# Optimization experiments

Measured on AMD Instinct MI355X. Metric: run time of the kernel, lower is better.

Reference implementation:

```python
import math
import jax, jax.numpy as jnp
import numpy as np

B, H, S, D = 2, 16, 2048, 1024
DK = D // H  # 64


def setup_inputs() -> dict:
    key = jax.random.key(0)
    k1, k2, k3, k4, k5 = jax.random.split(key, 5)
    scale = np.float32(0.02)
    return {
        "x": jax.random.normal(k1, (B, H, S, D), dtype=jnp.float32),
        "wq": jax.random.normal(k2, (DK, D), dtype=jnp.float32) * scale,
        "wk": jax.random.normal(k3, (DK, D), dtype=jnp.float32) * scale,
        "wv": jax.random.normal(k4, (DK, D), dtype=jnp.float32) * scale,
        "wo": jax.random.normal(k5, (D, D), dtype=jnp.float32) * scale,
    }


def reference(x, wq, wk, wv, wo):
    # x: [B, H, S, D]; wq/wk/wv: [dk, D]; wo: [D, D]
    b, h, s, d = x.shape
    xq = jnp.einsum("bhsd,kd->bhsk", x, wq)  # [B,H,S,dk]
    xk = jnp.einsum("bhsd,kd->bhsk", x, wk)
    xv = jnp.einsum("bhsd,kd->bhsk", x, wv)
    # NOTE: original scales by sqrt(hidden_dim), not sqrt(dk)
    inv_scale = np.float32(1.0 / math.sqrt(d))
    score = jnp.einsum("bhsk,bhtk->bhst", xq, xk) * inv_scale  # [B,H,S,S]
    attn = jax.nn.softmax(score, axis=-1).astype(xq.dtype)
    out = jnp.einsum("bhst,bhtk->bhsk", attn, xv)  # [B,H,S,dk]
    out = out.transpose(0, 2, 1, 3).reshape(b, s, h * (wq.shape[0]))  # [B,S,H*dk]
    return out @ wo.T  # [B,S,D]
```

## Files before the change

### kernel.cpp

```cpp
#include <hip/hip_runtime.h>
#include <math.h>

#define BB 2
#define HH 16
#define SS 2048
#define DD 1024
#define DK 64
#define BHS (BB*HH*SS)
#define QSCALE 0.04508422f

typedef short  bf16x8  __attribute__((ext_vector_type(8)));
typedef float  floatx4 __attribute__((ext_vector_type(4)));
typedef unsigned short u16;

#define MFMA(a,b,c) __builtin_amdgcn_mfma_f32_16x16x32_bf16((a),(b),(c),0,0,0)

__device__ __forceinline__ unsigned cvt_pk_bf16(float lo, float hi) {
    unsigned r;
    asm("v_cvt_pk_bf16_f32 %0, %1, %2" : "=v"(r) : "v"(lo), "v"(hi));
    return r;
}
__device__ __forceinline__ bf16x8 ldfrag(const u16* p) {
    union { uint4 u; bf16x8 b; } c;
    c.u = *(const uint4*)p;
    return c.b;
}
__device__ __forceinline__ void stbf4(u16* p, float4 t) {
    union { unsigned u[2]; uint2 v; } c;
    c.u[0] = cvt_pk_bf16(t.x, t.y);
    c.u[1] = cvt_pk_bf16(t.z, t.w);
    *(uint2*)p = c.v;
}
__device__ __forceinline__ void st4s(u16* p, float a, float b, float c, float d) {
    unsigned x = cvt_pk_bf16(a, b), y = cvt_pk_bf16(c, d);
    p[0]  = (u16)x; p[16] = (u16)(x >> 16);
    p[32] = (u16)y; p[48] = (u16)(y >> 16);
}

#define WQKV_CHUNKS (192*1024/4)
#define WO_CHUNKS   (1024*1024/4)
__global__ __launch_bounds__(256) void convert_w(
    const float* __restrict__ wq, const float* __restrict__ wk,
    const float* __restrict__ wv, const float* __restrict__ wo,
    u16* __restrict__ wqkv, u16* __restrict__ wo_bf)
{
    int i = blockIdx.x * 256 + threadIdx.x;
    if (i < WQKV_CHUNKS) {
        int r = i >> 8;
        int c = i & 255;
        const float* src = (r < 64) ? wq : ((r < 128) ? wk : wv);
        float4 t = *(const float4*)(src + (size_t)(r & 63) * DD + c * 4);
        stbf4(wqkv + (size_t)r * DD + c * 4, t);
    } else if (i < WQKV_CHUNKS + WO_CHUNKS) {
        int j = i - WQKV_CHUNKS;
        float4 t = *(const float4*)(wo + (size_t)j * 4);
        stbf4(wo_bf + (size_t)j * 4, t);
    }
}

__global__ __launch_bounds__(256) void qkv_proj(
    const float* __restrict__ x, const u16* __restrict__ wqkv,
    u16* __restrict__ q, u16* __restrict__ k, u16* __restrict__ vT)
{
    __shared__ __align__(16) u16 Xs[64][72];
    __shared__ __align__(16) u16 Ws[192][72];
    const int tid  = threadIdx.x;
    const int w    = tid >> 6;
    const int lane = tid & 63;
    const int quad = lane >> 4;
    const int l16  = lane & 15;
    const int rowbase = blockIdx.x * 64;

    floatx4 acc[12];
#pragma unroll
    for (int n = 0; n < 12; ++n) acc[n] = (floatx4){0.f,0.f,0.f,0.f};

    for (int k0 = 0; k0 < DD; k0 += 64) {
#pragma unroll
        for (int it = 0; it < 4; ++it) {
            int li = tid + it * 256;
            int r  = li >> 4;
            int c4 = li & 15;
            float4 t = *(const float4*)(x + (size_t)(rowbase + r) * DD + k0 + c4 * 4);
            stbf4(&Xs[r][c4 * 4], t);
        }
#pragma unroll
        for (int it = 0; it < 6; ++it) {
            int li = tid + it * 256;
            int r  = li >> 3;
            int c8 = li & 7;
            *(uint4*)&Ws[r][c8 * 8] =
                *(const uint4*)(wqkv + (size_t)r * DD + k0 + c8 * 8);
        }
        __syncthreads();

        bf16x8 a0 = ldfrag(&Xs[w * 16 + l16][quad * 8]);
        bf16x8 a1 = ldfrag(&Xs[w * 16 + l16][32 + quad * 8]);
#pragma unroll
        for (int n = 0; n < 12; ++n) {
            bf16x8 b0 = ldfrag(&Ws[n * 16 + l16][quad * 8]);
            bf16x8 b1 = ldfrag(&Ws[n * 16 + l16][32 + quad * 8]);
            acc[n] = MFMA(a0, b0, acc[n]);
            acc[n] = MFMA(a1, b1, acc[n]);
        }
        __syncthreads();
    }

#pragma unroll
    for (int r = 0; r < 4; ++r) {
        int row = w * 16 + quad * 4 + r;
        size_t m = (size_t)(rowbase + row);
        st4s(&q[m * DK + l16], acc[0][r] * QSCALE, acc[1][r] * QSCALE,
                               acc[2][r] * QSCALE, acc[3][r] * QSCALE);
        st4s(&k[m * DK + l16], acc[4][r], acc[5][r], acc[6][r], acc[7][r]);
    }
    u16 (*Vbuf)[72] = Xs;
#pragma unroll
    for (int r = 0; r < 4; ++r) {
        int row = w * 16 + quad * 4 + r;
        st4s(&Vbuf[row][l16], acc[8][r], acc[9][r], acc[10][r], acc[11][r]);
    }
    __syncthreads();
    {
        const int dk = tid >> 2;
        const int sc = (tid & 3) * 16;
        const int bh = rowbase >> 11;
        const int s0 = rowbase & 2047;
        union { u16 s[16]; uint4 u[2]; } t;
#pragma unroll
        for (int u = 0; u < 16; ++u) t.s[u] = Vbuf[sc + u][dk];
        uint4* dst = (uint4*)(vT + ((size_t)(bh * DK + dk)) * SS + s0 + sc);
        dst[0] = t.u[0];
        dst[1] = t.u[1];
    }
}

__global__ __launch_bounds__(256) void flash_attn(
    const u16* __restrict__ q, const u16* __restrict__ k,
    const u16* __restrict__ vT, u16* __restrict__ ao)
{
    __shared__ __align__(16) u16 Qs[64][72];
    __shared__ __align__(16) u16 Ks[64][72];
    __shared__ __align__(16) u16 Vt[64][72];
    __shared__ __align__(16) u16 Ps[4][16][72];
    const int tid  = threadIdx.x;
    const int w    = tid >> 6;
    const int lane = tid & 63;
    const int quad = lane >> 4;
    const int l16  = lane & 15;
    const int qt   = blockIdx.x;
    const int bh   = blockIdx.y;
    const size_t kbase = (size_t)bh * SS * DK;
    const size_t vbase = (size_t)bh * DK * SS;

#pragma unroll
    for (int it = 0; it < 2; ++it) {
        int li = tid + it * 256;
        int r  = li >> 3;
        int c8 = li & 7;
        *(uint4*)&Qs[r][c8 * 8] =
            *(const uint4*)(q + kbase + (size_t)(qt * 64 + r) * DK + c8 * 8);
    }

    float m_i[4], l_i[4];
    floatx4 acc_o[4];
#pragma unroll
    for (int r = 0; r < 4; ++r) { m_i[r] = -INFINITY; l_i[r] = 0.f; }
#pragma unroll
    for (int n = 0; n < 4; ++n) acc_o[n] = (floatx4){0.f,0.f,0.f,0.f};
    __syncthreads();

    for (int kt = 0; kt < SS / 64; ++kt) {
#pragma unroll
        for (int it = 0; it < 2; ++it) {
            int li = tid + it * 256;
            int r  = li >> 3;
            int c8 = li & 7;
            *(uint4*)&Ks[r][c8 * 8] =
                *(const uint4*)(k + kbase + (size_t)(kt * 64 + r) * DK + c8 * 8);
            *(uint4*)&Vt[r][c8 * 8] =
                *(const uint4*)(vT + vbase + (size_t)r * SS + kt * 64 + c8 * 8);
        }
        __syncthreads();

        floatx4 sc[4];
        __builtin_amdgcn_s_setprio(1);
        {
            bf16x8 a0 = ldfrag(&Qs[w * 16 + l16][quad * 8]);
            bf16x8 a1 = ldfrag(&Qs[w * 16 + l16][32 + quad * 8]);
#pragma unroll
            for (int n = 0; n < 4; ++n) {
                sc[n] = (floatx4){0.f,0.f,0.f,0.f};
                bf16x8 b0 = ldfrag(&Ks[n * 16 + l16][quad * 8]);
                bf16x8 b1 = ldfrag(&Ks[n * 16 + l16][32 + quad * 8]);
                sc[n] = MFMA(a0, b0, sc[n]);
                sc[n] = MFMA(a1, b1, sc[n]);
            }
        }
        __builtin_amdgcn_s_setprio(0);

        float rmx[4];
#pragma unroll
        for (int r = 0; r < 4; ++r) {
            float rm = fmaxf(fmaxf(sc[0][r], sc[1][r]), fmaxf(sc[2][r], sc[3][r]));
#pragma unroll
            for (int off = 1; off < 16; off <<= 1)
                rm = fmaxf(rm, __shfl_xor(rm, off, 64));
            rmx[r] = rm;
        }
        int ok = (rmx[0] <= m_i[0] + 8.f) & (rmx[1] <= m_i[1] + 8.f) &
                 (rmx[2] <= m_i[2] + 8.f) & (rmx[3] <= m_i[3] + 8.f);
        if (!__all(ok)) {
#pragma unroll
            for (int r = 0; r < 4; ++r) {
                float mnew  = fmaxf(m_i[r], rmx[r]);
                float alpha = __builtin_amdgcn_exp2f(m_i[r] - mnew);
#pragma unroll
                for (int n = 0; n < 4; ++n) acc_o[n][r] *= alpha;
                l_i[r] *= alpha;
                m_i[r]  = mnew;
            }
        }
#pragma unroll
        for (int r = 0; r < 4; ++r) {
            float mi = m_i[r];
            float p0 = __builtin_amdgcn_exp2f(sc[0][r] - mi);
            float p1 = __builtin_amdgcn_exp2f(sc[1][r] - mi);
            float p2 = __builtin_amdgcn_exp2f(sc[2][r] - mi);
            float p3 = __builtin_amdgcn_exp2f(sc[3][r] - mi);
            float rs = (p0 + p1) + (p2 + p3);
#pragma unroll
            for (int off = 1; off < 16; off <<= 1)
                rs += __shfl_xor(rs, off, 64);
            l_i[r] += rs;
            st4s(&Ps[w][quad * 4 + r][l16], p0, p1, p2, p3);
        }

        __builtin_amdgcn_s_setprio(1);
#pragma unroll
        for (int kc = 0; kc < 2; ++kc) {
            bf16x8 a = ldfrag(&Ps[w][l16][kc * 32 + quad * 8]);
#pragma unroll
            for (int n = 0; n < 4; ++n) {
                bf16x8 b = ldfrag(&Vt[n * 16 + l16][kc * 32 + quad * 8]);
                acc_o[n] = MFMA(a, b, acc_o[n]);
            }
        }
        __builtin_amdgcn_s_setprio(0);
        __syncthreads();
    }

    const int b = bh >> 4, h = bh & 15;
#pragma unroll
    for (int r = 0; r < 4; ++r) {
        int srow = qt * 64 + w * 16 + quad * 4 + r;
        float rl = __builtin_amdgcn_rcpf(l_i[r]);
        size_t base = ((size_t)(b * SS + srow)) * (HH * DK) + h * 64;
        st4s(&ao[base + l16], acc_o[0][r] * rl, acc_o[1][r] * rl,
                              acc_o[2][r] * rl, acc_o[3][r] * rl);
    }
}

__global__ __launch_bounds__(256) void out_proj(
    const u16* __restrict__ ao, const u16* __restrict__ wo_bf,
    float* __restrict__ out)
{
    __shared__ __align__(16) u16 As[64][72];
    __shared__ __align__(16) u16 Bs[64][72];
    const int tid  = threadIdx.x;
    const int w    = tid >> 6;
    const int lane = tid & 63;
    const int quad = lane >> 4;
    const int l16  = lane & 15;
    const int mt = blockIdx.y;
    const int nt = blockIdx.x;

    floatx4 acc[4];
#pragma unroll
    for (int n = 0; n < 4; ++n) acc[n] = (floatx4){0.f,0.f,0.f,0.f};

    for (int k0 = 0; k0 < DD; k0 += 64) {
#pragma unroll
        for (int it = 0; it < 2; ++it) {
            int li = tid + it * 256;
            int r  = li >> 3;
            int c8 = li & 7;
            *(uint4*)&As[r][c8 * 8] =
                *(const uint4*)(ao + (size_t)(mt * 64 + r) * DD + k0 + c8 * 8);
            *(uint4*)&Bs[r][c8 * 8] =
                *(const uint4*)(wo_bf + (size_t)(nt * 64 + r) * DD + k0 + c8 * 8);
        }
        __syncthreads();

        bf16x8 a0 = ldfrag(&As[w * 16 + l16][quad * 8]);
        bf16x8 a1 = ldfrag(&As[w * 16 + l16][32 + quad * 8]);
#pragma unroll
        for (int n = 0; n < 4; ++n) {
            bf16x8 b0 = ldfrag(&Bs[n * 16 + l16][quad * 8]);
            bf16x8 b1 = ldfrag(&Bs[n * 16 + l16][32 + quad * 8]);
            acc[n] = MFMA(a0, b0, acc[n]);
            acc[n] = MFMA(a1, b1, acc[n]);
        }
        __syncthreads();
    }

#pragma unroll
    for (int r = 0; r < 4; ++r) {
        int row = mt * 64 + w * 16 + quad * 4 + r;
#pragma unroll
        for (int n = 0; n < 4; ++n)
            out[(size_t)row * DD + nt * 64 + n * 16 + l16] = acc[n][r];
    }
}

extern "C" void kernel_launch(void* const* d_in, const int* in_sizes, int n_in,
                              void* d_out, int out_size, void* d_ws, size_t ws_size,
                              hipStream_t stream) {
    const float* x  = (const float*)d_in[0];
    const float* wq = (const float*)d_in[1];
    const float* wk = (const float*)d_in[2];
    const float* wv = (const float*)d_in[3];
    const float* wo = (const float*)d_in[4];
    float* out = (float*)d_out;

    u16* q    = (u16*)d_ws;
    u16* k    = q    + (size_t)BHS * DK;
    u16* vT   = k    + (size_t)BHS * DK;
    u16* ao   = vT   + (size_t)BHS * DK;
    u16* wqkv = ao   + (size_t)BHS * DK;
    u16* wo_bf = wqkv + (size_t)192 * DD;

    convert_w<<<dim3((WQKV_CHUNKS + WO_CHUNKS) / 256), dim3(256), 0, stream>>>(
        wq, wk, wv, wo, wqkv, wo_bf);
    qkv_proj<<<dim3(BHS / 64), dim3(256), 0, stream>>>(x, wqkv, q, k, vT);
    flash_attn<<<dim3(SS / 64, BB * HH), dim3(256), 0, stream>>>(q, k, vT, ao);
    out_proj<<<dim3(DD / 64, (BB * SS) / 64), dim3(256), 0, stream>>>(ao, wo_bf, out);
}
```

Before: 574.6 us.

## Double-buffer QKV projection, load x directly into registers, use 512 threads

```diff
diff --git a/kernel.cpp b/kernel.cpp
--- a/kernel.cpp
+++ b/kernel.cpp
@@ -35,6 +35,10 @@
     unsigned x = cvt_pk_bf16(a, b), y = cvt_pk_bf16(c, d);
     p[0]  = (u16)x; p[16] = (u16)(x >> 16);
     p[32] = (u16)y; p[48] = (u16)(y >> 16);
+}
+__device__ __forceinline__ void st2s(u16* p, float a, float b) {
+    unsigned x = cvt_pk_bf16(a, b);
+    p[0]  = (u16)x; p[16] = (u16)(x >> 16);
 }
 
 #define WQKV_CHUNKS (192*1024/4)
@@ -58,80 +62,109 @@
     }
 }
 
-__global__ __launch_bounds__(256) void qkv_proj(
+__global__ __launch_bounds__(512) void qkv_proj(
     const float* __restrict__ x, const u16* __restrict__ wqkv,
     u16* __restrict__ q, u16* __restrict__ k, u16* __restrict__ vT)
 {
-    __shared__ __align__(16) u16 Xs[64][72];
-    __shared__ __align__(16) u16 Ws[192][72];
+    __shared__ __align__(16) u16 Ws[2][192][72];
     const int tid  = threadIdx.x;
     const int w    = tid >> 6;
     const int lane = tid & 63;
     const int quad = lane >> 4;
     const int l16  = lane & 15;
+    const int rt   = w & 3;
+    const int g    = w >> 2;
     const int rowbase = blockIdx.x * 64;
-
-    floatx4 acc[12];
-#pragma unroll
-    for (int n = 0; n < 12; ++n) acc[n] = (floatx4){0.f,0.f,0.f,0.f};
-
-    for (int k0 = 0; k0 < DD; k0 += 64) {
-#pragma unroll
-        for (int it = 0; it < 4; ++it) {
-            int li = tid + it * 256;
-            int r  = li >> 4;
-            int c4 = li & 15;
-            float4 t = *(const float4*)(x + (size_t)(rowbase + r) * DD + k0 + c4 * 4);
-            stbf4(&Xs[r][c4 * 4], t);
-        }
-#pragma unroll
-        for (int it = 0; it < 6; ++it) {
-            int li = tid + it * 256;
-            int r  = li >> 3;
-            int c8 = li & 7;
-            *(uint4*)&Ws[r][c8 * 8] =
-                *(const uint4*)(wqkv + (size_t)r * DD + k0 + c8 * 8);
-        }
-        __syncthreads();
-
-        bf16x8 a0 = ldfrag(&Xs[w * 16 + l16][quad * 8]);
-        bf16x8 a1 = ldfrag(&Xs[w * 16 + l16][32 + quad * 8]);
-#pragma unroll
-        for (int n = 0; n < 12; ++n) {
-            bf16x8 b0 = ldfrag(&Ws[n * 16 + l16][quad * 8]);
-            bf16x8 b1 = ldfrag(&Ws[n * 16 + l16][32 + quad * 8]);
-            acc[n] = MFMA(a0, b0, acc[n]);
-            acc[n] = MFMA(a1, b1, acc[n]);
-        }
-        __syncthreads();
-    }
-
-#pragma unroll
-    for (int r = 0; r < 4; ++r) {
-        int row = w * 16 + quad * 4 + r;
-        size_t m = (size_t)(rowbase + row);
-        st4s(&q[m * DK + l16], acc[0][r] * QSCALE, acc[1][r] * QSCALE,
-                               acc[2][r] * QSCALE, acc[3][r] * QSCALE);
-        st4s(&k[m * DK + l16], acc[4][r], acc[5][r], acc[6][r], acc[7][r]);
-    }
-    u16 (*Vbuf)[72] = Xs;
-#pragma unroll
-    for (int r = 0; r < 4; ++r) {
-        int row = w * 16 + quad * 4 + r;
-        st4s(&Vbuf[row][l16], acc[8][r], acc[9][r], acc[10][r], acc[11][r]);
+    const float* xr = x + (size_t)(rowbase + rt * 16 + l16) * DD + quad * 8;
+
+    uint4 wreg[3];
+    auto wload = [&](int kk) {
+#pragma unroll
+        for (int it = 0; it < 3; ++it) {
+            int li = tid + it * 512;
+            int r  = li >> 3, c8 = li & 7;
+            wreg[it] = *(const uint4*)(wqkv + (size_t)r * DD + kk * 64 + c8 * 8);
+        }
+    };
+    auto wstore = [&](int p) {
+#pragma unroll
+        for (int it = 0; it < 3; ++it) {
+            int li = tid + it * 512;
+            int r  = li >> 3, c8 = li & 7;
+            *(uint4*)&Ws[p][r][c8 * 8] = wreg[it];
+        }
+    };
+
+    float4 xc[4], xn[4];
+    auto xload = [&](int kk, float4* d) {
+        const float* p = xr + kk * 64;
+        d[0] = *(const float4*)(p);
+        d[1] = *(const float4*)(p + 4);
+        d[2] = *(const float4*)(p + 32);
+        d[3] = *(const float4*)(p + 36);
+    };
+
+    floatx4 acc[6];
+#pragma unroll
+    for (int j = 0; j < 6; ++j) acc[j] = (floatx4){0.f,0.f,0.f,0.f};
+
+    wload(0); wstore(0);
+    xload(0, xc);
+    __syncthreads();
+
+    for (int kk = 0; kk < 16; ++kk) {
+        int p = kk & 1;
+        if (kk < 15) { wload(kk + 1); xload(kk + 1, xn); }
+        union { unsigned u[4]; bf16x8 v; } A0, A1;
+        A0.u[0] = cvt_pk_bf16(xc[0].x, xc[0].y);
+        A0.u[1] = cvt_pk_bf16(xc[0].z, xc[0].w);
+        A0.u[2] = cvt_pk_bf16(xc[1].x, xc[1].y);
+        A0.u[3] = cvt_pk_bf16(xc[1].z, xc[1].w);
+        A1.u[0] = cvt_pk_bf16(xc[2].x, xc[2].y);
+        A1.u[1] = cvt_pk_bf16(xc[2].z, xc[2].w);
+        A1.u[2] = cvt_pk_bf16(xc[3].x, xc[3].y);
+        A1.u[3] = cvt_pk_bf16(xc[3].z, xc[3].w);
+#pragma unroll
+        for (int j = 0; j < 6; ++j) {
+            int n = g * 6 + j;
+            bf16x8 b0 = ldfrag(&Ws[p][n * 16 + l16][quad * 8]);
+            bf16x8 b1 = ldfrag(&Ws[p][n * 16 + l16][32 + quad * 8]);
+            acc[j] = MFMA(A0.v, b0, acc[j]);
+            acc[j] = MFMA(A1.v, b1, acc[j]);
+        }
+        if (kk < 15) {
+            wstore(p ^ 1);
+#pragma unroll
+            for (int i2 = 0; i2 < 4; ++i2) xc[i2] = xn[i2];
+            __syncthreads();
+        }
+    }
+
+    u16 (*Vbuf)[72] = (u16 (*)[72])&Ws[0][0][0];
+#pragma unroll
+    for (int rr = 0; rr < 4; ++rr) {
+        int rloc = rt * 16 + quad * 4 + rr;
+        size_t m = (size_t)(rowbase + rloc);
+        if (g == 0) {
+            st4s(&q[m * DK + l16], acc[0][rr] * QSCALE, acc[1][rr] * QSCALE,
+                                   acc[2][rr] * QSCALE, acc[3][rr] * QSCALE);
+            st2s(&k[m * DK + l16], acc[4][rr], acc[5][rr]);
+        } else {
+            st2s(&k[m * DK + 32 + l16], acc[0][rr], acc[1][rr]);
+            st4s(&Vbuf[rloc][l16], acc[2][rr], acc[3][rr],
+                                   acc[4][rr], acc[5][rr]);
+        }
     }
     __syncthreads();
     {
-        const int dk = tid >> 2;
-        const int sc = (tid & 3) * 16;
+        const int dk = tid >> 3;
+        const int sc = (tid & 7) * 8;
         const int bh = rowbase >> 11;
         const int s0 = rowbase & 2047;
-        union { u16 s[16]; uint4 u[2]; } t;
-#pragma unroll
-        for (int u = 0; u < 16; ++u) t.s[u] = Vbuf[sc + u][dk];
-        uint4* dst = (uint4*)(vT + ((size_t)(bh * DK + dk)) * SS + s0 + sc);
-        dst[0] = t.u[0];
-        dst[1] = t.u[1];
+        union { u16 s[8]; uint4 u; } t;
+#pragma unroll
+        for (int u = 0; u < 8; ++u) t.s[u] = Vbuf[sc + u][dk];
+        *(uint4*)(vT + ((size_t)(bh * DK + dk)) * SS + s0 + sc) = t.u;
     }
 }
 
@@ -156,8 +189,7 @@
 #pragma unroll
     for (int it = 0; it < 2; ++it) {
         int li = tid + it * 256;
-        int r  = li >> 3;
-        int c8 = li & 7;
+        int r  = li >> 3, c8 = li & 7;
         *(uint4*)&Qs[r][c8 * 8] =
             *(const uint4*)(q + kbase + (size_t)(qt * 64 + r) * DK + c8 * 8);
     }
@@ -174,8 +206,7 @@
 #pragma unroll
         for (int it = 0; it < 2; ++it) {
             int li = tid + it * 256;
-            int r  = li >> 3;
-            int c8 = li & 7;
+            int r  = li >> 3, c8 = li & 7;
             *(uint4*)&Ks[r][c8 * 8] =
                 *(const uint4*)(k + kbase + (size_t)(kt * 64 + r) * DK + c8 * 8);
             *(uint4*)&Vt[r][c8 * 8] =
@@ -283,8 +314,7 @@
 #pragma unroll
         for (int it = 0; it < 2; ++it) {
             int li = tid + it * 256;
-            int r  = li >> 3;
-            int c8 = li & 7;
+            int r  = li >> 3, c8 = li & 7;
             *(uint4*)&As[r][c8 * 8] =
                 *(const uint4*)(ao + (size_t)(mt * 64 + r) * DD + k0 + c8 * 8);
             *(uint4*)&Bs[r][c8 * 8] =
@@ -323,16 +353,16 @@
     const float* wo = (const float*)d_in[4];
     float* out = (float*)d_out;
 
-    u16* q    = (u16*)d_ws;
-    u16* k    = q    + (size_t)BHS * DK;
-    u16* vT   = k    + (size_t)BHS * DK;
-    u16* ao   = vT   + (size_t)BHS * DK;
-    u16* wqkv = ao   + (size_t)BHS * DK;
+    u16* q     = (u16*)d_ws;
+    u16* k     = q    + (size_t)BHS * DK;
+    u16* vT    = k    + (size_t)BHS * DK;
+    u16* ao    = vT   + (size_t)BHS * DK;
+    u16* wqkv  = ao   + (size_t)BHS * DK;
     u16* wo_bf = wqkv + (size_t)192 * DD;
 
     convert_w<<<dim3((WQKV_CHUNKS + WO_CHUNKS) / 256), dim3(256), 0, stream>>>(
         wq, wk, wv, wo, wqkv, wo_bf);
-    qkv_proj<<<dim3(BHS / 64), dim3(256), 0, stream>>>(x, wqkv, q, k, vT);
+    qkv_proj<<<dim3(BHS / 64), dim3(512), 0, stream>>>(x, wqkv, q, k, vT);
     flash_attn<<<dim3(SS / 64, BB * HH), dim3(256), 0, stream>>>(q, k, vT, ao);
     out_proj<<<dim3(DD / 64, (BB * SS) / 64), dim3(256), 0, stream>>>(ao, wo_bf, out);
 }
```

Result: no change. 566.6 us (-1.4%).
